# Optimization experiments

Hardware: AMD Instinct MI355X
Metric: run time of the kernel (lower is better)

## Reference

```python
import jax, jax.numpy as jnp
import numpy as np

N_EMBED = 768
N_HEAD = 12
SEQ = 4096
BATCH = 1
LN_EPS = 1e-5


def setup_inputs() -> dict:
    key = jax.random.key(0)
    ks = jax.random.split(key, 12)
    d = N_EMBED
    s = 0.02
    return {
        "x": jax.random.normal(ks[0], (BATCH, SEQ, d), jnp.float32),
        "w_qkv": jax.random.normal(ks[1], (d, 3 * d), jnp.float32) * s,
        "b_qkv": jnp.zeros((3 * d,), jnp.float32),
        "w_proj": jax.random.normal(ks[2], (d, d), jnp.float32) * s,
        "b_proj": jnp.zeros((d,), jnp.float32),
        "w_fc1": jax.random.normal(ks[3], (d, 4 * d), jnp.float32) * s,
        "b_fc1": jnp.zeros((4 * d,), jnp.float32),
        "w_fc2": jax.random.normal(ks[4], (4 * d, d), jnp.float32) * s,
        "b_fc2": jnp.zeros((d,), jnp.float32),
        "ln1_g": jnp.ones((d,), jnp.float32),
        "ln1_b": jnp.zeros((d,), jnp.float32),
        "ln2_g": jnp.ones((d,), jnp.float32),
        "ln2_b": jnp.zeros((d,), jnp.float32),
    }


def _layernorm(x, g, b):
    mu = jnp.mean(x, axis=-1, keepdims=True)
    var = jnp.mean(jnp.square(x - mu), axis=-1, keepdims=True)
    return (x - mu) * jax.lax.rsqrt(var + LN_EPS) * g + b


def _attn(x, w_qkv, b_qkv, w_proj, b_proj):
    B, S, D = x.shape
    hd = D // N_HEAD
    kqv = x @ w_qkv + b_qkv
    # torch order: k, q, v
    k, q, v = jnp.split(kqv, 3, axis=-1)
    def heads(t):
        return t.reshape(B, S, N_HEAD, hd).transpose(0, 2, 1, 3)  # [B,H,S,hd]
    k, q, v = heads(k), heads(q), heads(v)
    scores = jnp.einsum("bhqd,bhkd->bhqk", q, k) * (1.0 / jnp.sqrt(jnp.float32(hd)))
    causal = jnp.tril(jnp.ones((S, S), bool))
    scores = jnp.where(causal, scores, -jnp.inf)
    attn = jax.nn.softmax(scores, axis=-1)
    # dropout is identity in eval mode
    y = jnp.einsum("bhqk,bhkd->bhqd", attn, v)
    y = y.transpose(0, 2, 1, 3).reshape(B, S, D)
    return y @ w_proj + b_proj


def reference(x, w_qkv, b_qkv, w_proj, b_proj, w_fc1, b_fc1, w_fc2, b_fc2,
              ln1_g, ln1_b, ln2_g, ln2_b):
    x = x + _attn(_layernorm(x, ln1_g, ln1_b), w_qkv, b_qkv, w_proj, b_proj)
    h = _layernorm(x, ln2_g, ln2_b)
    h = jax.nn.gelu(h @ w_fc1 + b_fc1, approximate=False)
    return x + (h @ w_fc2 + b_fc2)
```

## Files before the change

kernel.cpp:

```cpp
#include <hip/hip_runtime.h>
#include <hip/hip_bf16.h>

#define S_LEN 4096
#define D_EMB 768
#define NH    12
#define HD    64
#define DQKV  2304
#define DFF   3072

typedef __attribute__((ext_vector_type(4))) short short4v;
typedef __attribute__((ext_vector_type(8))) short short8v;
typedef __attribute__((ext_vector_type(4))) float float4v;

static __device__ __forceinline__ float4v mfma16(short4v a, short4v b, float4v c) {
  return __builtin_amdgcn_mfma_f32_16x16x16bf16_1k(a, b, c, 0, 0, 0);
}

static __device__ __forceinline__ short bf16bits(float f) {
  __hip_bfloat16 h = __float2bfloat16(f);
  return *reinterpret_cast<short*>(&h);
}

static __device__ __forceinline__ float fast_exp2(float x) {
#if __has_builtin(__builtin_amdgcn_exp2f)
  return __builtin_amdgcn_exp2f(x);
#else
  return exp2f(x);
#endif
}

static __device__ __forceinline__ void gload16(const __hip_bfloat16* g, __hip_bfloat16* l) {
  __builtin_amdgcn_global_load_lds((const __attribute__((address_space(1))) void*)g,
                                   (__attribute__((address_space(3))) void*)l, 16, 0, 0);
}

__global__ __launch_bounds__(256) void ln_kernel(const float* __restrict__ x,
    const float* __restrict__ g, const float* __restrict__ b,
    __hip_bfloat16* __restrict__ out)
{
  int row = blockIdx.x;
  int tid = threadIdx.x;
  const float* xr = x + (size_t)row * D_EMB;
  float v0 = xr[tid], v1 = xr[tid + 256], v2 = xr[tid + 512];
  float s  = v0 + v1 + v2;
  float sq = v0 * v0 + v1 * v1 + v2 * v2;
  #pragma unroll
  for (int off = 32; off >= 1; off >>= 1) {
    s  += __shfl_xor(s, off);
    sq += __shfl_xor(sq, off);
  }
  __shared__ float ss[4], ssq[4];
  if ((tid & 63) == 0) { ss[tid >> 6] = s; ssq[tid >> 6] = sq; }
  __syncthreads();
  s  = ss[0] + ss[1] + ss[2] + ss[3];
  sq = ssq[0] + ssq[1] + ssq[2] + ssq[3];
  float mean = s * (1.0f / D_EMB);
  float var  = sq * (1.0f / D_EMB) - mean * mean;
  float rstd = rsqrtf(var + 1e-5f);
  __hip_bfloat16* orow = out + (size_t)row * D_EMB;
  orow[tid]       = __float2bfloat16((v0 - mean) * rstd * g[tid]       + b[tid]);
  orow[tid + 256] = __float2bfloat16((v1 - mean) * rstd * g[tid + 256] + b[tid + 256]);
  orow[tid + 512] = __float2bfloat16((v2 - mean) * rstd * g[tid + 512] + b[tid + 512]);
}

__global__ __launch_bounds__(256) void transpose_bf16_kernel(const float* __restrict__ in,
    __hip_bfloat16* __restrict__ out, int K, int N)
{
  __shared__ float t[32][33];
  int nb = N >> 5;
  int bn = blockIdx.x % nb, bk = blockIdx.x / nb;
  int tx = threadIdx.x & 31, ty = threadIdx.x >> 5;
  #pragma unroll
  for (int i = 0; i < 4; i++)
    t[ty + 8 * i][tx] = in[(size_t)(bk * 32 + ty + 8 * i) * N + bn * 32 + tx];
  __syncthreads();
  #pragma unroll
  for (int i = 0; i < 4; i++)
    out[(size_t)(bn * 32 + ty + 8 * i) * K + bk * 32 + tx] = __float2bfloat16(t[tx][ty + 8 * i]);
}

__global__ __launch_bounds__(256) void vt_kernel(const __hip_bfloat16* __restrict__ kqv,
                                                 __hip_bfloat16* __restrict__ vT)
{
  __shared__ __hip_bfloat16 t[32][33];
  int bs = blockIdx.x & 127;
  int bd = blockIdx.x >> 7;
  int tx = threadIdx.x & 31, ty = threadIdx.x >> 5;
  #pragma unroll
  for (int i = 0; i < 4; i++)
    t[ty + 8 * i][tx] = kqv[(size_t)(bs * 32 + ty + 8 * i) * DQKV + 2 * D_EMB + bd * 32 + tx];
  __syncthreads();
  #pragma unroll
  for (int i = 0; i < 4; i++)
    vT[(size_t)(bd * 32 + ty + 8 * i) * S_LEN + bs * 32 + tx] = t[tx][ty + 8 * i];
}

template<int EPI>
__global__ __launch_bounds__(256) void gemm_kernel(
    const __hip_bfloat16* __restrict__ A,
    const __hip_bfloat16* __restrict__ Bt,
    const float* __restrict__ bias,
    const float* __restrict__ resid,
    void* __restrict__ Cout,
    int M, int N, int Kfull, int kChunk)
{
  __shared__ __hip_bfloat16 Asm[128 * 64];
  __shared__ __hip_bfloat16 Bsm[128 * 64];
  int nb = N >> 7, mb = M >> 7;
  int tilesPer = nb * mb;
  int split = blockIdx.x / tilesPer;
  int b2 = blockIdx.x % tilesPer;
  int bx = b2 % nb, by = b2 / nb;
  int m0 = by << 7, n0 = bx << 7;
  int k0 = split * kChunk;
  int tid = threadIdx.x;
  int lane = tid & 63, lg = lane >> 4, li = lane & 15;
  int w = tid >> 6, wr = w >> 1, wc = w & 1;

  int sr  = tid >> 3;
  int scn = (tid & 7) ^ (sr & 7);
  const __hip_bfloat16* aSrc = A  + (size_t)(m0 + sr) * Kfull + k0 + scn * 8;
  const __hip_bfloat16* bSrc = Bt + (size_t)(n0 + sr) * Kfull + k0 + scn * 8;
  __hip_bfloat16* aDst = Asm + tid * 8;
  __hip_bfloat16* bDst = Bsm + tid * 8;
  const size_t rowStep = (size_t)32 * Kfull;

  float4v acc[4][4];
  #pragma unroll
  for (int i = 0; i < 4; i++)
    #pragma unroll
    for (int j = 0; j < 4; j++) {
      float4v z = {0.f, 0.f, 0.f, 0.f};
      acc[i][j] = z;
    }

  int sw = li & 7;

  for (int kt = 0; kt < kChunk; kt += 64) {
    #pragma unroll
    for (int i = 0; i < 4; i++) {
      gload16(aSrc + i * rowStep, aDst + i * 2048);
      gload16(bSrc + i * rowStep, bDst + i * 2048);
    }
    aSrc += 64; bSrc += 64;
    __syncthreads();
    #pragma unroll
    for (int kk = 0; kk < 2; kk++) {
      short8v af[4], bf[4];
      #pragma unroll
      for (int f = 0; f < 4; f++) {
        int ar = wr * 64 + f * 16 + li;
        int br = wc * 64 + f * 16 + li;
        int ch = ((kk << 2) | lg) ^ sw;
        af[f] = *(const short8v*)(Asm + ar * 64 + ch * 8);
        bf[f] = *(const short8v*)(Bsm + br * 64 + ch * 8);
      }
      #pragma unroll
      for (int fr = 0; fr < 4; fr++)
        #pragma unroll
        for (int fc = 0; fc < 4; fc++)
          acc[fr][fc] = __builtin_amdgcn_mfma_f32_16x16x32_bf16(af[fr], bf[fc], acc[fr][fc], 0, 0, 0);
    }
    __syncthreads();
  }

  #pragma unroll
  for (int fr = 0; fr < 4; fr++) {
    int row = m0 + wr * 64 + fr * 16 + lg * 4;
    #pragma unroll
    for (int fc = 0; fc < 4; fc++) {
      int col = n0 + wc * 64 + fc * 16 + li;
      float bv = (EPI == 3) ? 0.f : bias[col];
      #pragma unroll
      for (int r = 0; r < 4; r++) {
        float v = acc[fr][fc][r] + bv;
        size_t idx = (size_t)(row + r) * N + col;
        if (EPI == 1) {
          float u = 0.7978845608028654f * (v + 0.044715f * v * v * v);
          float e = fast_exp2(u * 2.8853900817779268f);
#if __has_builtin(__builtin_amdgcn_rcpf)
          float r1 = __builtin_amdgcn_rcpf(e + 1.0f);
#else
          float r1 = 1.0f / (e + 1.0f);
#endif
          v = v * e * r1;
          ((__hip_bfloat16*)Cout)[idx] = __float2bfloat16(v);
        } else if (EPI == 2) {
          ((float*)Cout)[idx] = v + resid[idx];
        } else if (EPI == 3) {
          ((float*)Cout)[(size_t)split * M * N + idx] = v;
        } else {
          ((__hip_bfloat16*)Cout)[idx] = __float2bfloat16(v);
        }
      }
    }
  }
}

template<int NS>
__global__ __launch_bounds__(256) void reduce_kernel(const float* __restrict__ parts,
    const float* __restrict__ bias, const float* __restrict__ resid,
    float* __restrict__ out, int n4)
{
  int stride = gridDim.x * 256;
  for (int e = blockIdx.x * 256 + threadIdx.x; e < n4; e += stride) {
    float4v acc = *(const float4v*)(resid + 4 * (size_t)e);
    int col = (e * 4) % D_EMB;
    float4v bv = *(const float4v*)(bias + col);
    acc += bv;
    #pragma unroll
    for (int s = 0; s < NS; s++)
      acc += *(const float4v*)(parts + (size_t)s * 4 * n4 + 4 * (size_t)e);
    *(float4v*)(out + 4 * (size_t)e) = acc;
  }
}

__global__ __launch_bounds__(256) void reduce_ln_kernel(const float* __restrict__ parts,
    const float* __restrict__ bias, const float* __restrict__ resid,
    const float* __restrict__ g, const float* __restrict__ b,
    float* __restrict__ x1, __hip_bfloat16* __restrict__ lnout)
{
  const size_t MN = (size_t)S_LEN * D_EMB;
  int row = blockIdx.x;
  int tid = threadIdx.x;
  float v[3];
  float s = 0.f, sq = 0.f;
  #pragma unroll
  for (int i = 0; i < 3; i++) {
    int col = tid + i * 256;
    size_t idx = (size_t)row * D_EMB + col;
    float a = resid[idx] + bias[col] + parts[idx] + parts[idx + MN] + parts[idx + 2 * MN];
    x1[idx] = a;
    v[i] = a;
    s += a;
    sq += a * a;
  }
  #pragma unroll
  for (int off = 32; off >= 1; off >>= 1) {
    s  += __shfl_xor(s, off);
    sq += __shfl_xor(sq, off);
  }
  __shared__ float ss[4], ssq[4];
  if ((tid & 63) == 0) { ss[tid >> 6] = s; ssq[tid >> 6] = sq; }
  __syncthreads();
  s  = ss[0] + ss[1] + ss[2] + ss[3];
  sq = ssq[0] + ssq[1] + ssq[2] + ssq[3];
  float mean = s * (1.0f / D_EMB);
  float var  = sq * (1.0f / D_EMB) - mean * mean;
  float rstd = rsqrtf(var + 1e-5f);
  __hip_bfloat16* orow = lnout + (size_t)row * D_EMB;
  #pragma unroll
  for (int i = 0; i < 3; i++) {
    int col = tid + i * 256;
    orow[col] = __float2bfloat16((v[i] - mean) * rstd * g[col] + b[col]);
  }
}

#define SCL_LOG2E 0.18033688011f
template<bool SPLIT>
__global__ __launch_bounds__(512, 4) void attn_kernel(const __hip_bfloat16* __restrict__ kqv,
                                                      const __hip_bfloat16* __restrict__ vT,
                                                      __hip_bfloat16* __restrict__ y,
                                                      char* __restrict__ partial)
{
  __shared__ __hip_bfloat16 Ksm[2][64 * 64];
  __shared__ __hip_bfloat16 Vtsm[2][64 * 64];

  int bid = blockIdx.x;
  int h, gi, c;
  if (SPLIT) {
    int task = (bid >> 3) + (bid & 7) * 60;
    h = task / 40;
    int t = task % 40;
    if      (t < 16) { gi = 15 - (t >> 2);        c = t & 3; }
    else if (t < 28) { gi = 11 - (t - 16) / 3;    c = (t - 16) % 3; }
    else if (t < 36) { gi = 7  - ((t - 28) >> 1); c = (t - 28) & 1; }
    else             { gi = 3  - (t - 36);        c = 0; }
  } else {
    h = bid / 16; gi = 15 - (bid % 16); c = 0;
  }
  int ntile = 4 * gi + 4;
  int kt0 = c << 4;
  int kt1 = SPLIT ? min(kt0 + 16, ntile) : ntile;
  bool direct = SPLIT ? (gi < 4) : true;

  int tid = threadIdx.x;
  int w = tid >> 6, lane = tid & 63, lg = lane >> 4, li = lane & 15;
  int sw = li & 7;
  int qb0 = gi * 256 + w * 16;

  int ksr  = tid >> 3;
  int kscn = (tid & 7) ^ (ksr & 7);
  const __hip_bfloat16* kSrc0 = kqv + h * HD + (size_t)ksr * DQKV + kscn * 8;
  const __hip_bfloat16* vSrc0 = vT + (size_t)(h * HD + ksr) * S_LEN + kscn * 8;
  const size_t kTileStep = (size_t)64 * DQKV;

  short8v q8[2][2];
  #pragma unroll
  for (int g = 0; g < 2; g++) {
    const __hip_bfloat16* qp = kqv + (size_t)(qb0 + g * 128 + li) * DQKV + D_EMB + h * HD + 8 * lg;
    q8[g][0] = *(const short8v*)(qp);
    q8[g][1] = *(const short8v*)(qp + 32);
  }

  const short4v ones4 = { (short)0x3F80, (short)0x3F80, (short)0x3F80, (short)0x3F80 };
  float4v ol0 = {0.f,0.f,0.f,0.f}, ol1 = {0.f,0.f,0.f,0.f};
  float4v o0[4], o1[4];
  #pragma unroll
  for (int fc = 0; fc < 4; fc++) { float4v z = {0.f,0.f,0.f,0.f}; o0[fc] = z; o1[fc] = z; }

  gload16(kSrc0 + (size_t)kt0 * kTileStep, Ksm[0] + tid * 8);
  gload16(vSrc0 + (size_t)kt0 * 64,        Vtsm[0] + tid * 8);

  for (int kb = kt0; kb < kt1; kb++) {
    int p = kb & 1;
    __syncthreads();
    if (kb + 1 < kt1) {
      gload16(kSrc0 + (size_t)(kb + 1) * kTileStep, Ksm[p ^ 1] + tid * 8);
      gload16(vSrc0 + (size_t)(kb + 1) * 64,        Vtsm[p ^ 1] + tid * 8);
    }

    bool act0 = (kb * 64 <= qb0 + 15);
    bool act1 = (kb * 64 <= qb0 + 128 + 15);
    if (!act1) continue;

    float4v s0[4], s1[4];
    #pragma unroll
    for (int fc = 0; fc < 4; fc++) { float4v z = {0.f,0.f,0.f,0.f}; s0[fc] = z; s1[fc] = z; }
    #pragma unroll
    for (int kk = 0; kk < 2; kk++) {
      #pragma unroll
      for (int fc = 0; fc < 4; fc++) {
        int ch = ((kk << 2) | lg) ^ sw;
        short8v kf = *(const short8v*)(Ksm[p] + (fc * 16 + li) * 64 + ch * 8);
        s0[fc] = __builtin_amdgcn_mfma_f32_16x16x32_bf16(kf, q8[0][kk], s0[fc], 0, 0, 0);
        s1[fc] = __builtin_amdgcn_mfma_f32_16x16x32_bf16(kf, q8[1][kk], s1[fc], 0, 0, 0);
      }
    }

    if (act0) {
      bool needmask = (kb * 64 + 63 > qb0);
      if (needmask) {
        #pragma unroll
        for (int fc = 0; fc < 4; fc++) {
          #pragma unroll
          for (int rr = 0; rr < 4; rr++) {
            float pv = fast_exp2(s0[fc][rr] * SCL_LOG2E);
            if ((kb * 64 + fc * 16 + 4 * lg + rr) > (qb0 + li)) pv = 0.f;
            s0[fc][rr] = pv;
          }
        }
      } else {
        #pragma unroll
        for (int fc = 0; fc < 4; fc++) {
          #pragma unroll
          for (int rr = 0; rr < 4; rr++)
            s0[fc][rr] = fast_exp2(s0[fc][rr] * SCL_LOG2E);
        }
      }
    }

    {
      int qb1 = qb0 + 128;
      bool needmask = (kb * 64 + 63 > qb1);
      if (needmask) {
        #pragma unroll
        for (int fc = 0; fc < 4; fc++) {
          #pragma unroll
          for (int rr = 0; rr < 4; rr++) {
            float pv = fast_exp2(s1[fc][rr] * SCL_LOG2E);
            if ((kb * 64 + fc * 16 + 4 * lg + rr) > (qb1 + li)) pv = 0.f;
            s1[fc][rr] = pv;
          }
        }
      } else {
        #pragma unroll
        for (int fc = 0; fc < 4; fc++) {
          #pragma unroll
          for (int rr = 0; rr < 4; rr++)
            s1[fc][rr] = fast_exp2(s1[fc][rr] * SCL_LOG2E);
        }
      }
    }

    if (act0) {
      #pragma unroll
      for (int kk = 0; kk < 4; kk++) {
        short4v pb0, pb1;
        #pragma unroll
        for (int rr = 0; rr < 4; rr++) { pb0[rr] = bf16bits(s0[kk][rr]); pb1[rr] = bf16bits(s1[kk][rr]); }
        ol0 = mfma16(ones4, pb0, ol0);
        ol1 = mfma16(ones4, pb1, ol1);
        int c2 = (kk << 1) | (lg >> 1);
        #pragma unroll
        for (int fc = 0; fc < 4; fc++) {
          short4v vf = *(const short4v*)(Vtsm[p] + (fc * 16 + li) * 64 + ((c2 ^ sw) << 3) + 4 * (lg & 1));
          o0[fc] = mfma16(vf, pb0, o0[fc]);
          o1[fc] = mfma16(vf, pb1, o1[fc]);
        }
      }
    } else {
      #pragma unroll
      for (int kk = 0; kk < 4; kk++) {
        short4v pb1;
        #pragma unroll
        for (int rr = 0; rr < 4; rr++) pb1[rr] = bf16bits(s1[kk][rr]);
        ol1 = mfma16(ones4, pb1, ol1);
        int c2 = (kk << 1) | (lg >> 1);
        #pragma unroll
        for (int fc = 0; fc < 4; fc++) {
          short4v vf = *(const short4v*)(Vtsm[p] + (fc * 16 + li) * 64 + ((c2 ^ sw) << 3) + 4 * (lg & 1));
          o1[fc] = mfma16(vf, pb1, o1[fc]);
        }
      }
    }
  }

  if (direct) {
    float inv0 = 1.0f / ol0[0], inv1 = 1.0f / ol1[0];
    int q0 = qb0 + li;
    #pragma unroll
    for (int fc = 0; fc < 4; fc++) {
      short4v ov0, ov1;
      #pragma unroll
      for (int rr = 0; rr < 4; rr++) { ov0[rr] = bf16bits(o0[fc][rr] * inv0); ov1[rr] = bf16bits(o1[fc][rr] * inv1); }
      *reinterpret_cast<short4v*>(y + (size_t)q0 * D_EMB + h * HD + fc * 16 + 4 * lg) = ov0;
      *reinterpret_cast<short4v*>(y + (size_t)(q0 + 128) * D_EMB + h * HD + fc * 16 + 4 * lg) = ov1;
    }
  } else {
    int offg = (gi < 8) ? (gi - 4) * 2 : (gi < 12) ? 8 + (gi - 8) * 3 : 20 + (gi - 12) * 4;
    char* slot = partial + (size_t)(h * 36 + offg + c) * 33792;
    int q = (w & 3) * 16 + li;
    #pragma unroll
    for (int g = 0; g < 2; g++) {
      char* ps = slot + (size_t)(g * 2 + (w >> 2)) * 8448;
      __hip_bfloat16* pO = (__hip_bfloat16*)ps;
      float* pL = (float*)(ps + 8192);
      #pragma unroll
      for (int fc = 0; fc < 4; fc++) {
        #pragma unroll
        for (int rr = 0; rr < 4; rr++) {
          float val = g ? o1[fc][rr] : o0[fc][rr];
          pO[(fc * 16 + 4 * lg + rr) * 64 + q] = __float2bfloat16(val);
        }
      }
      if (lg == 0) pL[q] = g ? ol1[0] : ol0[0];
    }
  }
}

__global__ __launch_bounds__(256) void attn_combine_kernel(const char* __restrict__ partial,
                                                           __hip_bfloat16* __restrict__ y)
{
  int task = blockIdx.x;
  int h  = task / 48;
  int qb = 16 + task % 48;
  int gi = qb >> 2, slab = qb & 3;
  int nch = (gi >> 2) + 1;
  int offg = (gi < 8) ? (gi - 4) * 2 : (gi < 12) ? 8 + (gi - 8) * 3 : 20 + (gi - 12) * 4;
  const char* base = partial + (size_t)(h * 36 + offg) * 33792 + (size_t)slab * 8448;
  int wv = threadIdx.x >> 6;
  int lane = threadIdx.x & 63;

  float L = 0.f;
  float acc[16];
  #pragma unroll
  for (int j = 0; j < 16; j++) acc[j] = 0.f;
  #pragma unroll
  for (int c = 0; c < 4; c++) {
    if (c < nch) {
      const char* cb = base + (size_t)c * 33792;
      L += ((const float*)(cb + 8192))[lane];
      const __hip_bfloat16* O = (const __hip_bfloat16*)cb;
      #pragma unroll
      for (int j = 0; j < 16; j++)
        acc[j] += __bfloat162float(O[(wv * 16 + j) * 64 + lane]);
    }
  }
  float inv = 1.0f / L;
  __hip_bfloat16* yp = y + (size_t)(qb * 64 + lane) * D_EMB + h * HD + wv * 16;
  short8v a0, a1;
  #pragma unroll
  for (int j = 0; j < 8; j++) a0[j] = bf16bits(acc[j] * inv);
  #pragma unroll
  for (int j = 0; j < 8; j++) a1[j] = bf16bits(acc[8 + j] * inv);
  *reinterpret_cast<short8v*>(yp)     = a0;
  *reinterpret_cast<short8v*>(yp + 8) = a1;
}

extern "C" void kernel_launch(void* const* d_in, const int* in_sizes, int n_in,
                              void* d_out, int out_size, void* d_ws, size_t ws_size,
                              hipStream_t stream)
{
  const float* x      = (const float*)d_in[0];
  const float* w_qkv  = (const float*)d_in[1];
  const float* b_qkv  = (const float*)d_in[2];
  const float* w_proj = (const float*)d_in[3];
  const float* b_proj = (const float*)d_in[4];
  const float* w_fc1  = (const float*)d_in[5];
  const float* b_fc1  = (const float*)d_in[6];
  const float* w_fc2  = (const float*)d_in[7];
  const float* b_fc2  = (const float*)d_in[8];
  const float* ln1_g  = (const float*)d_in[9];
  const float* ln1_b  = (const float*)d_in[10];
  const float* ln2_g  = (const float*)d_in[11];
  const float* ln2_b  = (const float*)d_in[12];

  char* ws = (char*)d_ws;
  size_t off = 0;
  __hip_bfloat16* wqkvT = (__hip_bfloat16*)(ws + off); off += (size_t)DQKV * D_EMB * 2;
  __hip_bfloat16* wprojT= (__hip_bfloat16*)(ws + off); off += (size_t)D_EMB * D_EMB * 2;
  __hip_bfloat16* wfc1T = (__hip_bfloat16*)(ws + off); off += (size_t)DFF * D_EMB * 2;
  __hip_bfloat16* wfc2T = (__hip_bfloat16*)(ws + off); off += (size_t)D_EMB * DFF * 2;
  __hip_bfloat16* lnbuf = (__hip_bfloat16*)(ws + off); off += (size_t)S_LEN * D_EMB * 2;
  __hip_bfloat16* kqv   = (__hip_bfloat16*)(ws + off);
  __hip_bfloat16* hbuf  = kqv;                         off += (size_t)S_LEN * DQKV * 2;
  __hip_bfloat16* ybuf  = (__hip_bfloat16*)(ws + off); off += (size_t)S_LEN * D_EMB * 2;
  __hip_bfloat16* vTbuf = (__hip_bfloat16*)(ws + off); off += (size_t)S_LEN * D_EMB * 2;
  float*          x1    = (float*)(ws + off);          off += (size_t)S_LEN * D_EMB * 4;
  char*           part  = ws + off;
  size_t needSplit = off + (size_t)4 * S_LEN * D_EMB * 4;
  size_t needAttn  = off + (size_t)432 * 33792;
  bool splitk  = (ws_size >= needSplit);
  bool attnSpl = (ws_size >= needAttn);
  const int MN4 = S_LEN * D_EMB / 4;
  (void)in_sizes; (void)n_in; (void)out_size;

  transpose_bf16_kernel<<<dim3((DQKV/32)*(D_EMB/32)), dim3(256), 0, stream>>>(w_qkv,  wqkvT, D_EMB, DQKV);
  transpose_bf16_kernel<<<dim3((D_EMB/32)*(D_EMB/32)), dim3(256), 0, stream>>>(w_proj, wprojT, D_EMB, D_EMB);
  transpose_bf16_kernel<<<dim3((DFF/32)*(D_EMB/32)),   dim3(256), 0, stream>>>(w_fc1,  wfc1T, D_EMB, DFF);
  transpose_bf16_kernel<<<dim3((D_EMB/32)*(DFF/32)),   dim3(256), 0, stream>>>(w_fc2,  wfc2T, DFF, D_EMB);

  ln_kernel<<<dim3(S_LEN), dim3(256), 0, stream>>>(x, ln1_g, ln1_b, lnbuf);
  gemm_kernel<0><<<dim3((DQKV/128)*(S_LEN/128)), dim3(256), 0, stream>>>(
      lnbuf, wqkvT, b_qkv, nullptr, kqv, S_LEN, DQKV, D_EMB, D_EMB);
  vt_kernel<<<dim3(128 * 24), dim3(256), 0, stream>>>(kqv, vTbuf);

  if (attnSpl) {
    attn_kernel<true><<<dim3(480), dim3(512), 0, stream>>>(kqv, vTbuf, ybuf, part);
    attn_combine_kernel<<<dim3(576), dim3(256), 0, stream>>>(part, ybuf);
  } else {
    attn_kernel<false><<<dim3(192), dim3(512), 0, stream>>>(kqv, vTbuf, ybuf, part);
  }

  if (splitk) {
    gemm_kernel<3><<<dim3((D_EMB/128)*(S_LEN/128)*3), dim3(256), 0, stream>>>(
        ybuf, wprojT, nullptr, nullptr, (float*)part, S_LEN, D_EMB, D_EMB, D_EMB/3);
    reduce_ln_kernel<<<dim3(S_LEN), dim3(256), 0, stream>>>(
        (float*)part, b_proj, x, ln2_g, ln2_b, x1, lnbuf);
  } else {
    gemm_kernel<2><<<dim3((D_EMB/128)*(S_LEN/128)), dim3(256), 0, stream>>>(
        ybuf, wprojT, b_proj, x, x1, S_LEN, D_EMB, D_EMB, D_EMB);
    ln_kernel<<<dim3(S_LEN), dim3(256), 0, stream>>>(x1, ln2_g, ln2_b, lnbuf);
  }

  gemm_kernel<1><<<dim3((DFF/128)*(S_LEN/128)), dim3(256), 0, stream>>>(
      lnbuf, wfc1T, b_fc1, nullptr, hbuf, S_LEN, DFF, D_EMB, D_EMB);

  if (splitk) {
    gemm_kernel<3><<<dim3((D_EMB/128)*(S_LEN/128)*4), dim3(256), 0, stream>>>(
        hbuf, wfc2T, nullptr, nullptr, (float*)part, S_LEN, D_EMB, DFF, DFF/4);
    reduce_kernel<4><<<dim3(1024), dim3(256), 0, stream>>>(
        (float*)part, b_fc2, x1, (float*)d_out, MN4);
  } else {
    gemm_kernel<2><<<dim3((D_EMB/128)*(S_LEN/128)), dim3(256), 0, stream>>>(
        hbuf, wfc2T, b_fc2, x1, (float*)d_out, S_LEN, D_EMB, DFF, DFF);
  }
}
```

Measured before the change: 199.6 us.

## Fuse V transpose into QKV GEMM epilogue and store split-K partials in bf16

The QKV GEMM epilogue now also writes the V columns transposed into the vT buffer, so the separate vt_kernel launch is removed. Split-K partial sums for the projection and FC2 GEMMs are stored as bf16 instead of fp32, and the reduce kernels widen them back to float, halving partial-buffer traffic. The bf16 partials lose precision before the residual add. The transposed V stores are 8-byte writes strided by the sequence length, which may be poorly coalesced.

New measurement: 188.1 us. 1.06x faster.

```diff
diff --git a/kernel.cpp b/kernel.cpp
--- a/kernel.cpp
+++ b/kernel.cpp
@@ -79,22 +79,6 @@
     out[(size_t)(bn * 32 + ty + 8 * i) * K + bk * 32 + tx] = __float2bfloat16(t[tx][ty + 8 * i]);
 }
 
-__global__ __launch_bounds__(256) void vt_kernel(const __hip_bfloat16* __restrict__ kqv,
-                                                 __hip_bfloat16* __restrict__ vT)
-{
-  __shared__ __hip_bfloat16 t[32][33];
-  int bs = blockIdx.x & 127;
-  int bd = blockIdx.x >> 7;
-  int tx = threadIdx.x & 31, ty = threadIdx.x >> 5;
-  #pragma unroll
-  for (int i = 0; i < 4; i++)
-    t[ty + 8 * i][tx] = kqv[(size_t)(bs * 32 + ty + 8 * i) * DQKV + 2 * D_EMB + bd * 32 + tx];
-  __syncthreads();
-  #pragma unroll
-  for (int i = 0; i < 4; i++)
-    vT[(size_t)(bd * 32 + ty + 8 * i) * S_LEN + bs * 32 + tx] = t[tx][ty + 8 * i];
-}
-
 template<int EPI>
 __global__ __launch_bounds__(256) void gemm_kernel(
     const __hip_bfloat16* __restrict__ A,
@@ -102,6 +86,7 @@
     const float* __restrict__ bias,
     const float* __restrict__ resid,
     void* __restrict__ Cout,
+    __hip_bfloat16* __restrict__ vtout,
     int M, int N, int Kfull, int kChunk)
 {
   __shared__ __hip_bfloat16 Asm[128 * 64];
@@ -171,6 +156,7 @@
     for (int fc = 0; fc < 4; fc++) {
       int col = n0 + wc * 64 + fc * 16 + li;
       float bv = (EPI == 3) ? 0.f : bias[col];
+      short4v tv;
       #pragma unroll
       for (int r = 0; r < 4; r++) {
         float v = acc[fr][fc][r] + bv;
@@ -188,20 +174,26 @@
         } else if (EPI == 2) {
           ((float*)Cout)[idx] = v + resid[idx];
         } else if (EPI == 3) {
-          ((float*)Cout)[(size_t)split * M * N + idx] = v;
+          ((__hip_bfloat16*)Cout)[(size_t)split * M * N + idx] = __float2bfloat16(v);
         } else {
-          ((__hip_bfloat16*)Cout)[idx] = __float2bfloat16(v);
-        }
+          __hip_bfloat16 hb = __float2bfloat16(v);
+          ((__hip_bfloat16*)Cout)[idx] = hb;
+          if (EPI == 4) tv[r] = *reinterpret_cast<short*>(&hb);
+        }
+      }
+      if (EPI == 4 && col >= 2 * D_EMB) {
+        *reinterpret_cast<short4v*>(vtout + (size_t)(col - 2 * D_EMB) * S_LEN + row) = tv;
       }
     }
   }
 }
 
 template<int NS>
-__global__ __launch_bounds__(256) void reduce_kernel(const float* __restrict__ parts,
+__global__ __launch_bounds__(256) void reduce_kernel(const __hip_bfloat16* __restrict__ parts,
     const float* __restrict__ bias, const float* __restrict__ resid,
     float* __restrict__ out, int n4)
 {
+  const size_t MN = (size_t)S_LEN * D_EMB;
   int stride = gridDim.x * 256;
   for (int e = blockIdx.x * 256 + threadIdx.x; e < n4; e += stride) {
     float4v acc = *(const float4v*)(resid + 4 * (size_t)e);
@@ -209,13 +201,19 @@
     float4v bv = *(const float4v*)(bias + col);
     acc += bv;
     #pragma unroll
-    for (int s = 0; s < NS; s++)
-      acc += *(const float4v*)(parts + (size_t)s * 4 * n4 + 4 * (size_t)e);
+    for (int s = 0; s < NS; s++) {
+      short4v pv = *(const short4v*)(parts + (size_t)s * MN + 4 * (size_t)e);
+      #pragma unroll
+      for (int j = 0; j < 4; j++) {
+        unsigned int u = ((unsigned int)(unsigned short)pv[j]) << 16;
+        acc[j] += *reinterpret_cast<float*>(&u);
+      }
+    }
     *(float4v*)(out + 4 * (size_t)e) = acc;
   }
 }
 
-__global__ __launch_bounds__(256) void reduce_ln_kernel(const float* __restrict__ parts,
+__global__ __launch_bounds__(256) void reduce_ln_kernel(const __hip_bfloat16* __restrict__ parts,
     const float* __restrict__ bias, const float* __restrict__ resid,
     const float* __restrict__ g, const float* __restrict__ b,
     float* __restrict__ x1, __hip_bfloat16* __restrict__ lnout)
@@ -229,7 +227,10 @@
   for (int i = 0; i < 3; i++) {
     int col = tid + i * 256;
     size_t idx = (size_t)row * D_EMB + col;
-    float a = resid[idx] + bias[col] + parts[idx] + parts[idx + MN] + parts[idx + 2 * MN];
+    float a = resid[idx] + bias[col]
+            + __bfloat162float(parts[idx])
+            + __bfloat162float(parts[idx + MN])
+            + __bfloat162float(parts[idx + 2 * MN]);
     x1[idx] = a;
     v[i] = a;
     s += a;
@@ -519,7 +520,7 @@
   __hip_bfloat16* vTbuf = (__hip_bfloat16*)(ws + off); off += (size_t)S_LEN * D_EMB * 2;
   float*          x1    = (float*)(ws + off);          off += (size_t)S_LEN * D_EMB * 4;
   char*           part  = ws + off;
-  size_t needSplit = off + (size_t)4 * S_LEN * D_EMB * 4;
+  size_t needSplit = off + (size_t)4 * S_LEN * D_EMB * 2;
   size_t needAttn  = off + (size_t)432 * 33792;
   bool splitk  = (ws_size >= needSplit);
   bool attnSpl = (ws_size >= needAttn);
@@ -532,9 +533,8 @@
   transpose_bf16_kernel<<<dim3((D_EMB/32)*(DFF/32)),   dim3(256), 0, stream>>>(w_fc2,  wfc2T, DFF, D_EMB);
 
   ln_kernel<<<dim3(S_LEN), dim3(256), 0, stream>>>(x, ln1_g, ln1_b, lnbuf);
-  gemm_kernel<0><<<dim3((DQKV/128)*(S_LEN/128)), dim3(256), 0, stream>>>(
-      lnbuf, wqkvT, b_qkv, nullptr, kqv, S_LEN, DQKV, D_EMB, D_EMB);
-  vt_kernel<<<dim3(128 * 24), dim3(256), 0, stream>>>(kqv, vTbuf);
+  gemm_kernel<4><<<dim3((DQKV/128)*(S_LEN/128)), dim3(256), 0, stream>>>(
+      lnbuf, wqkvT, b_qkv, nullptr, kqv, vTbuf, S_LEN, DQKV, D_EMB, D_EMB);
 
   if (attnSpl) {
     attn_kernel<true><<<dim3(480), dim3(512), 0, stream>>>(kqv, vTbuf, ybuf, part);
@@ -545,25 +545,25 @@
 
   if (splitk) {
     gemm_kernel<3><<<dim3((D_EMB/128)*(S_LEN/128)*3), dim3(256), 0, stream>>>(
-        ybuf, wprojT, nullptr, nullptr, (float*)part, S_LEN, D_EMB, D_EMB, D_EMB/3);
+        ybuf, wprojT, nullptr, nullptr, part, nullptr, S_LEN, D_EMB, D_EMB, D_EMB/3);
     reduce_ln_kernel<<<dim3(S_LEN), dim3(256), 0, stream>>>(
-        (float*)part, b_proj, x, ln2_g, ln2_b, x1, lnbuf);
+        (const __hip_bfloat16*)part, b_proj, x, ln2_g, ln2_b, x1, lnbuf);
   } else {
     gemm_kernel<2><<<dim3((D_EMB/128)*(S_LEN/128)), dim3(256), 0, stream>>>(
-        ybuf, wprojT, b_proj, x, x1, S_LEN, D_EMB, D_EMB, D_EMB);
+        ybuf, wprojT, b_proj, x, x1, nullptr, S_LEN, D_EMB, D_EMB, D_EMB);
     ln_kernel<<<dim3(S_LEN), dim3(256), 0, stream>>>(x1, ln2_g, ln2_b, lnbuf);
   }
 
   gemm_kernel<1><<<dim3((DFF/128)*(S_LEN/128)), dim3(256), 0, stream>>>(
-      lnbuf, wfc1T, b_fc1, nullptr, hbuf, S_LEN, DFF, D_EMB, D_EMB);
+      lnbuf, wfc1T, b_fc1, nullptr, hbuf, nullptr, S_LEN, DFF, D_EMB, D_EMB);
 
   if (splitk) {
     gemm_kernel<3><<<dim3((D_EMB/128)*(S_LEN/128)*4), dim3(256), 0, stream>>>(
-        hbuf, wfc2T, nullptr, nullptr, (float*)part, S_LEN, D_EMB, DFF, DFF/4);
+        hbuf, wfc2T, nullptr, nullptr, part, nullptr, S_LEN, D_EMB, DFF, DFF/4);
     reduce_kernel<4><<<dim3(1024), dim3(256), 0, stream>>>(
-        (float*)part, b_fc2, x1, (float*)d_out, MN4);
+        (const __hip_bfloat16*)part, b_fc2, x1, (float*)d_out, MN4);
   } else {
     gemm_kernel<2><<<dim3((D_EMB/128)*(S_LEN/128)), dim3(256), 0, stream>>>(
-        hbuf, wfc2T, b_fc2, x1, (float*)d_out, S_LEN, D_EMB, DFF, DFF);
-  }
-}
+        hbuf, wfc2T, b_fc2, x1, (float*)d_out, nullptr, S_LEN, D_EMB, DFF, DFF);
+  }
+}
```
